# Performance work log

Measured on AMD Instinct MI355X. Metric: run time of the kernel, lower is better.

## Reference

```python
import jax, jax.numpy as jnp
import numpy as np

INNER_DIM = 256
DT_SIZE = 64
STATE_DIM = 256  # must equal INNER_DIM for the original split() to be valid
BATCH, SEQ_LEN = 2, 512


def setup_inputs() -> dict:
    key = jax.random.key(0)
    k_x, k_win, k_wdt, k_bdt = jax.random.split(key, 4)
    x = jax.random.normal(k_x, (BATCH, SEQ_LEN, INNER_DIM), dtype=jnp.float32)
    # nn.Linear(inner_dim, dt_size + 2*state_dim, bias=False); stored as [in, out] for x @ W
    W_in = jax.random.normal(k_win, (INNER_DIM, DT_SIZE + 2 * STATE_DIM), dtype=jnp.float32) / np.sqrt(INNER_DIM)
    # nn.Linear(dt_size, inner_dim) with bias
    W_dt = jax.random.normal(k_wdt, (DT_SIZE, INNER_DIM), dtype=jnp.float32) / np.sqrt(DT_SIZE)
    b_dt = jax.random.normal(k_bdt, (INNER_DIM,), dtype=jnp.float32) * 0.01
    # alpha_log = log(repeat(arange(1, N+1), 'n -> d n'))
    alpha_log = jnp.log(jnp.broadcast_to(
        jnp.arange(1, STATE_DIM + 1, dtype=jnp.float32), (INNER_DIM, STATE_DIM)))
    delta = jnp.ones((INNER_DIM,), dtype=jnp.float32)
    return {"input_tensor": x, "W_in": W_in, "W_dt": W_dt, "b_dt": b_dt,
            "alpha_log": alpha_log, "delta": delta}


def reference(input_tensor, W_in, W_dt, b_dt, alpha_log, delta):
    x = input_tensor
    alpha = -jnp.exp(alpha_log)  # [D, N]
    proj = x @ W_in  # [B, L, DT + 2D]
    dt_raw, beta, gamma = jnp.split(proj, [DT_SIZE, DT_SIZE + INNER_DIM], axis=-1)
    dt = jax.nn.softplus(dt_raw @ W_dt + b_dt)  # [B, L, D]
    # dt_a = exp(dt[...,None] * alpha) : [B, L, D, N]
    dt_a = jnp.exp(jnp.einsum('bld,dn->bldn', dt, alpha))
    # dt_b_i = dt * x outer beta : [B, L, D, N]
    dt_b_i = jnp.einsum('bld,bln->bldn', dt * x, beta)

    def step(state, inputs):
        a_t, b_t, g_t = inputs  # [B,D,N], [B,D,N], [B,N]
        state = a_t * state + b_t
        y_t = jnp.einsum('bdn,bn->bd', state, g_t)
        return state, y_t

    s0 = jnp.zeros((x.shape[0], INNER_DIM, STATE_DIM), dtype=x.dtype)
    _, ys = jax.lax.scan(step, s0, (jnp.moveaxis(dt_a, 1, 0),
                                    jnp.moveaxis(dt_b_i, 1, 0),
                                    jnp.moveaxis(gamma, 1, 0)))
    ys = jnp.moveaxis(ys, 0, 1)  # [B, L, D]
    return ys + x * delta
```

## Files before the change

kernel.cpp:

```cpp
#include <hip/hip_runtime.h>
#include <math.h>

#define DIM   256
#define NST   256
#define LSEQ  512
#define BAT   2
#define DTSZ  64
#define PCOLS 576
#define NROWS 1024

constexpr float LOG2E = 1.4426950408889634f;

__device__ __forceinline__ float fexp2(float v) {
#if __has_builtin(__builtin_amdgcn_exp2f)
    return __builtin_amdgcn_exp2f(v);
#else
    return exp2f(v);
#endif
}

__device__ __forceinline__ float softplusf(float v) {
    return (v > 20.f) ? v : log1pf(__expf(v));
}

__device__ __forceinline__ void barrier_lds_only() {
    __builtin_amdgcn_s_waitcnt(0xC07F);
    __builtin_amdgcn_s_barrier();
}

__device__ __forceinline__ unsigned pack_bg(float be, float ga) {
    unsigned ub = __float_as_uint(be);
    unsigned ug = __float_as_uint(ga);
    ub = (ub + 0x7fffu + ((ub >> 16) & 1u)) >> 16;
    ug = (ug + 0x7fffu + ((ug >> 16) & 1u)) & 0xffff0000u;
    return ub | ug;
}

__global__ __launch_bounds__(256) void proj_kernel(
    const float* __restrict__ x, const float* __restrict__ W_in,
    const float* __restrict__ W_dt, const float* __restrict__ b_dt,
    unsigned* __restrict__ betgam,
    float* __restrict__ dtp, float* __restrict__ dtxp)
{
    __shared__ float xs[2][DIM];
    __shared__ float draw[2][DTSZ];
    const int j = threadIdx.x;
    const int row0 = blockIdx.x * 2;

    #pragma unroll
    for (int r = 0; r < 2; ++r) xs[r][j] = x[(row0 + r) * DIM + j];
    __syncthreads();

    float acc0[2] = {0.f, 0.f}, acc1[2] = {0.f, 0.f}, acc2[2] = {0.f, 0.f};
    const bool has2 = (j < 64);

    for (int kk = 0; kk < DIM; kk += 16) {
        float w0[16], w1[16], w2[16];
        #pragma unroll
        for (int u = 0; u < 16; ++u) {
            const int k = kk + u;
            w0[u] = W_in[k * PCOLS + j];
            w1[u] = W_in[k * PCOLS + 256 + j];
            w2[u] = has2 ? W_in[k * PCOLS + 512 + j] : 0.f;
        }
        #pragma unroll
        for (int r = 0; r < 2; ++r) {
            #pragma unroll
            for (int q = 0; q < 4; ++q) {
                float4 xv = *(const float4*)&xs[r][kk + q * 4];
                const float xa[4] = {xv.x, xv.y, xv.z, xv.w};
                #pragma unroll
                for (int u = 0; u < 4; ++u) {
                    const int uu = q * 4 + u;
                    acc0[r] = fmaf(xa[u], w0[uu], acc0[r]);
                    acc1[r] = fmaf(xa[u], w1[uu], acc1[r]);
                    acc2[r] = fmaf(xa[u], w2[uu], acc2[r]);
                }
            }
        }
    }

    #pragma unroll
    for (int r = 0; r < 2; ++r) {
        const int row = row0 + r;
        if (has2) {
            draw[r][j] = acc0[r];
            betgam[row * NST + 192 + j] = pack_bg(acc1[r], acc2[r]);
        } else {
            betgam[row * NST + (j - 64)] = pack_bg(acc0[r], acc1[r]);
        }
    }
    __syncthreads();

    float bd = b_dt[j];
    float accd[2] = {bd, bd};
    #pragma unroll 16
    for (int k = 0; k < DTSZ; ++k) {
        float w = W_dt[k * DIM + j];
        #pragma unroll
        for (int r = 0; r < 2; ++r) accd[r] = fmaf(draw[r][k], w, accd[r]);
    }
    #pragma unroll
    for (int r = 0; r < 2; ++r) {
        const int row = row0 + r;
        float sp = softplusf(accd[r]);
        dtp[row * DIM + j]  = sp;
        dtxp[row * DIM + j] = sp * xs[r][j];
    }
}

__global__ __launch_bounds__(256, 2) void scan1p(
    const float* __restrict__ x,
    const float* __restrict__ alpha_log,
    const float* __restrict__ delta,
    const unsigned* __restrict__ betgam,
    const float* __restrict__ dtp,
    const float* __restrict__ dtxp,
    float* __restrict__ out)
{
    __shared__ float part[32][NST];
    __shared__ float dts[LSEQ], dxs[LSEQ], xcol[LSEQ];
    const int n = threadIdx.x;
    const int xcd  = blockIdx.x & 7;
    const int slot = blockIdx.x >> 3;
    const int b = xcd >> 2;
    const int d = slot * 4 + (xcd & 3);
    const int rb = b * LSEQ;

    #pragma unroll
    for (int it = 0; it < 2; ++it) {
        const int l = n + it * 256;
        dts[l]  = dtp [(rb + l) * DIM + d];
        dxs[l]  = dtxp[(rb + l) * DIM + d];
        xcol[l] = x   [(rb + l) * DIM + d];
    }
    const float aln = -__expf(alpha_log[d * NST + n]) * LOG2E;
    const float dv  = delta[d];
    __syncthreads();

    float s = 0.f;
    unsigned bg[8][8];
    #pragma unroll
    for (int pw = 0; pw < 6; ++pw) {
        #pragma unroll
        for (int t = 0; t < 8; ++t)
            bg[pw][t] = betgam[(rb + pw * 8 + t) * NST + n];
    }

    #pragma unroll 8
    for (int w = 0; w < 64; ++w) {
        const int cur = w & 7;
        const int pf  = (w + 6) & 7;
        if (w + 6 < 64) {
            #pragma unroll
            for (int t = 0; t < 8; ++t)
                bg[pf][t] = betgam[(rb + (w + 6) * 8 + t) * NST + n];
        }
        float4 dta = *(const float4*)&dts[w * 8];
        float4 dtb = *(const float4*)&dts[w * 8 + 4];
        float4 dxa = *(const float4*)&dxs[w * 8];
        float4 dxb = *(const float4*)&dxs[w * 8 + 4];
        const float dtw[8] = {dta.x, dta.y, dta.z, dta.w, dtb.x, dtb.y, dtb.z, dtb.w};
        const float dxw[8] = {dxa.x, dxa.y, dxa.z, dxa.w, dxb.x, dxb.y, dxb.z, dxb.w};

        const int prow = (w & 3) * 8;
        #pragma unroll
        for (int t = 0; t < 8; ++t) {
            const unsigned u = bg[cur][t];
            const float be = __uint_as_float(u << 16);
            const float ga = __uint_as_float(u & 0xffff0000u);
            float a = fexp2(dtw[t] * aln);
            s = fmaf(a, s, dxw[t] * be);
            part[prow + t][n] = s * ga;
        }

        if ((w & 3) == 3) {
            barrier_lds_only();
            const int trow = n >> 3, seg = n & 7;
            float sum = 0.f;
            #pragma unroll
            for (int k = 0; k < 32; ++k)
                sum += part[trow][seg * 32 + ((k + n) & 31)];
            sum += __shfl_xor(sum, 1);
            sum += __shfl_xor(sum, 2);
            sum += __shfl_xor(sum, 4);
            if (seg == 0) {
                const int l = (w >> 2) * 32 + trow;
                out[(rb + l) * DIM + d] = sum + xcol[l] * dv;
            }
            barrier_lds_only();
        }
    }
}

extern "C" void kernel_launch(void* const* d_in, const int* in_sizes, int n_in,
                              void* d_out, int out_size, void* d_ws, size_t ws_size,
                              hipStream_t stream) {
    const float* x         = (const float*)d_in[0];
    const float* W_in      = (const float*)d_in[1];
    const float* W_dt      = (const float*)d_in[2];
    const float* b_dt      = (const float*)d_in[3];
    const float* alpha_log = (const float*)d_in[4];
    const float* delta     = (const float*)d_in[5];
    float* out = (float*)d_out;

    unsigned* betgam = (unsigned*)d_ws;
    float* dtp  = (float*)(betgam + NROWS * NST);
    float* dtxp = dtp + NROWS * DIM;

    proj_kernel<<<NROWS / 2, 256, 0, stream>>>(x, W_in, W_dt, b_dt, betgam, dtp, dtxp);
    scan1p<<<BAT * DIM, 256, 0, stream>>>(x, alpha_log, delta, betgam, dtp, dtxp, out);
}
```

Measured before the change: 119.6 us.

## Transpose packed beta/gamma so scan threads load contiguous uint4 timesteps

Adds a transpose kernel that rewrites the packed bf16 beta/gamma buffer from [row][n] to [n][row] layout. Each scan thread can then fetch eight consecutive timesteps with two 16-byte loads instead of eight strided 4-byte loads, and the prefetch ring shrinks from 8x8 registers to 4x2 uint4. The cost is an extra kernel launch plus a 1 MB read/write pass over the buffer. Per-instruction loads are no longer coalesced across the wavefront, since each lane reads a different n row.

```diff
diff --git a/kernel.cpp b/kernel.cpp
--- a/kernel.cpp
+++ b/kernel.cpp
@@ -109,11 +109,33 @@
     }
 }
 
+__global__ __launch_bounds__(256) void transp_kernel(
+    const unsigned* __restrict__ bg, unsigned* __restrict__ bgT)
+{
+    __shared__ unsigned tile[16][257];
+    const int t = threadIdx.x;
+    const int row0 = blockIdx.x * 16;
+    #pragma unroll
+    for (int r = 0; r < 16; ++r) tile[r][t] = bg[(row0 + r) * NST + t];
+    __syncthreads();
+    const int g = t & 3, nb = t >> 2;
+    #pragma unroll
+    for (int nn = 0; nn < 4; ++nn) {
+        const int n = nb + 64 * nn;
+        uint4 v;
+        v.x = tile[g * 4 + 0][n];
+        v.y = tile[g * 4 + 1][n];
+        v.z = tile[g * 4 + 2][n];
+        v.w = tile[g * 4 + 3][n];
+        *(uint4*)&bgT[(size_t)n * NROWS + row0 + g * 4] = v;
+    }
+}
+
 __global__ __launch_bounds__(256, 2) void scan1p(
     const float* __restrict__ x,
     const float* __restrict__ alpha_log,
     const float* __restrict__ delta,
-    const unsigned* __restrict__ betgam,
+    const unsigned* __restrict__ betgamT,
     const float* __restrict__ dtp,
     const float* __restrict__ dtxp,
     float* __restrict__ out)
@@ -138,23 +160,23 @@
     const float dv  = delta[d];
     __syncthreads();
 
+    const unsigned* bgp = betgamT + (size_t)n * NROWS + rb;
+
     float s = 0.f;
-    unsigned bg[8][8];
-    #pragma unroll
-    for (int pw = 0; pw < 6; ++pw) {
-        #pragma unroll
-        for (int t = 0; t < 8; ++t)
-            bg[pw][t] = betgam[(rb + pw * 8 + t) * NST + n];
-    }
-
-    #pragma unroll 8
+    uint4 bg4[4][2];
+    #pragma unroll
+    for (int pw = 0; pw < 3; ++pw) {
+        bg4[pw][0] = *(const uint4*)&bgp[pw * 8];
+        bg4[pw][1] = *(const uint4*)&bgp[pw * 8 + 4];
+    }
+
+    #pragma unroll 4
     for (int w = 0; w < 64; ++w) {
-        const int cur = w & 7;
-        const int pf  = (w + 6) & 7;
-        if (w + 6 < 64) {
-            #pragma unroll
-            for (int t = 0; t < 8; ++t)
-                bg[pf][t] = betgam[(rb + (w + 6) * 8 + t) * NST + n];
+        const int cur = w & 3;
+        const int pf  = (w + 3) & 3;
+        if (w + 3 < 64) {
+            bg4[pf][0] = *(const uint4*)&bgp[(w + 3) * 8];
+            bg4[pf][1] = *(const uint4*)&bgp[(w + 3) * 8 + 4];
         }
         float4 dta = *(const float4*)&dts[w * 8];
         float4 dtb = *(const float4*)&dts[w * 8 + 4];
@@ -162,11 +184,13 @@
         float4 dxb = *(const float4*)&dxs[w * 8 + 4];
         const float dtw[8] = {dta.x, dta.y, dta.z, dta.w, dtb.x, dtb.y, dtb.z, dtb.w};
         const float dxw[8] = {dxa.x, dxa.y, dxa.z, dxa.w, dxb.x, dxb.y, dxb.z, dxb.w};
+        const unsigned bgw[8] = {bg4[cur][0].x, bg4[cur][0].y, bg4[cur][0].z, bg4[cur][0].w,
+                                 bg4[cur][1].x, bg4[cur][1].y, bg4[cur][1].z, bg4[cur][1].w};
 
         const int prow = (w & 3) * 8;
         #pragma unroll
         for (int t = 0; t < 8; ++t) {
-            const unsigned u = bg[cur][t];
+            const unsigned u = bgw[t];
             const float be = __uint_as_float(u << 16);
             const float ga = __uint_as_float(u & 0xffff0000u);
             float a = fexp2(dtw[t] * aln);
@@ -204,10 +228,12 @@
     const float* delta     = (const float*)d_in[5];
     float* out = (float*)d_out;
 
-    unsigned* betgam = (unsigned*)d_ws;
-    float* dtp  = (float*)(betgam + NROWS * NST);
+    unsigned* betgam  = (unsigned*)d_ws;
+    unsigned* betgamT = betgam + NROWS * NST;
+    float* dtp  = (float*)(betgamT + NROWS * NST);
     float* dtxp = dtp + NROWS * DIM;
 
     proj_kernel<<<NROWS / 2, 256, 0, stream>>>(x, W_in, W_dt, b_dt, betgam, dtp, dtxp);
-    scan1p<<<BAT * DIM, 256, 0, stream>>>(x, alpha_log, delta, betgam, dtp, dtxp, out);
-}
+    transp_kernel<<<NROWS / 16, 256, 0, stream>>>(betgam, betgamT);
+    scan1p<<<BAT * DIM, 256, 0, stream>>>(x, alpha_log, delta, betgamT, dtp, dtxp, out);
+}
```

New measurement: 128.2 us. 1.07x slower.
